# Kernel optimization log

Measured on AMD Instinct MI355X. Metric: run time of the kernel, lower is better.

The kernel has to match this reference:

```python
import jax, jax.numpy as jnp
import numpy as np

B = 2097152  # number of Gaussians


def setup_inputs() -> dict:
    key = jax.random.key(0)
    k1, k2, k3, k4, k5, k6 = jax.random.split(key, 6)
    return {
        "loc1": jax.random.normal(k1, (B, 3), dtype=jnp.float32),
        "scale1": jax.random.uniform(k2, (B, 3), dtype=jnp.float32),
        "rot_matrix1": jax.random.normal(k3, (B, 3, 3), dtype=jnp.float32),
        "loc2": jax.random.normal(k4, (B, 3), dtype=jnp.float32),
        "scale2": jax.random.uniform(k5, (B, 3), dtype=jnp.float32),
        "rot_matrix2": jax.random.normal(k6, (B, 3, 3), dtype=jnp.float32),
    }


def reference(loc1, scale1, rot_matrix1, loc2, scale2, rot_matrix2):
    # ||mu1 - mu2||^2  -> (B,)
    loc_diff2 = jnp.sum((loc1 - loc2) ** 2, axis=-1)

    # cov2 = R2 diag(scale2) R2^T  -> (B,3,3)
    cov2 = jnp.einsum("bij,bj,bkj->bik", rot_matrix2, scale2, rot_matrix2)
    # cov2 rotated into frame of Gaussian 1: R1^T cov2 R1  -> (B,3,3)
    cov2_R1 = jnp.einsum("bji,bjk,bkl->bil", rot_matrix1, cov2, rot_matrix1)

    # E = diag(sqrt(s1)) cov2_R1 diag(sqrt(s1)), then symmetrize
    s1_sqrt = jnp.sqrt(scale1)  # (B,3)
    E = s1_sqrt[:, :, None] * cov2_R1 * s1_sqrt[:, None, :]
    E = (E + jnp.swapaxes(E, 1, 2)) * 0.5

    # trace of matrix sqrt via eigenvalues: sum (lambda^2)^(1/4) = sum |lambda|^(1/2)
    E_eig = jnp.linalg.eigvalsh(E)  # (B,3)
    E_sqrt_trace = jnp.sum(jnp.sqrt(jnp.sqrt(E_eig ** 2)), axis=-1)

    cov_wasserstein = jnp.sum(scale1, axis=-1) + jnp.sum(scale2, axis=-1) - 2.0 * E_sqrt_trace
    cov_wasserstein = jnp.maximum(cov_wasserstein, 0.0)
    return jnp.sqrt(loc_diff2 + cov_wasserstein)
```

## Files before the change

### kernel.cpp

```cpp
#include <hip/hip_runtime.h>
#include <math.h>

#define BLK 256

typedef __attribute__((address_space(1))) void gvoid_t;
typedef __attribute__((address_space(3))) void lvoid_t;

__device__ __forceinline__ void lds_dma16(const float* gsrc, float* ldst) {
    __builtin_amdgcn_global_load_lds((gvoid_t*)gsrc, (lvoid_t*)ldst, 16, 0, 0);
}
__device__ __forceinline__ void lds_dma4(const float* gsrc, float* ldst) {
    __builtin_amdgcn_global_load_lds((gvoid_t*)gsrc, (lvoid_t*)ldst, 4, 0, 0);
}

struct F3 { float x, y, z; };

__global__ __launch_bounds__(BLK, 8) void wasserstein_kernel(
    const float* __restrict__ loc1,   const float* __restrict__ scale1,
    const float* __restrict__ rot1,   const float* __restrict__ loc2,
    const float* __restrict__ scale2, const float* __restrict__ rot2,
    float* __restrict__ out)
{
    __shared__ __align__(16) float smem[4 * 1152];

    const int tid  = threadIdx.x;
    const int lane = tid & 63;
    const int wave = tid >> 6;
    const long long blockStart = (long long)blockIdx.x * BLK;
    const long long waveStart  = blockStart + (long long)(wave * 64);

    float* wR1 = smem + wave * 1152;
    float* wR2 = wR1 + 576;

    {
        const float* g1 = rot1 + waveStart * 9;
        const float* g2 = rot2 + waveStart * 9;
        lds_dma16(g1 + lane * 4,       wR1);
        lds_dma16(g1 + 256 + lane * 4, wR1 + 256);
        lds_dma4 (g1 + 512 + lane,     wR1 + 512);
        lds_dma16(g2 + lane * 4,       wR2);
        lds_dma16(g2 + 256 + lane * 4, wR2 + 256);
        lds_dma4 (g2 + 512 + lane,     wR2 + 512);
    }

    const long long i = blockStart + tid;
    const F3 L1 = *reinterpret_cast<const F3*>(loc1   + i * 3);
    const F3 L2 = *reinterpret_cast<const F3*>(loc2   + i * 3);
    const F3 S1 = *reinterpret_cast<const F3*>(scale1 + i * 3);
    const F3 S2 = *reinterpret_cast<const F3*>(scale2 + i * 3);

    const float dx = L1.x - L2.x, dy = L1.y - L2.y, dz = L1.z - L2.z;
    const float loc_diff2 = dx * dx + dy * dy + dz * dz;
    const float s1a = S1.x, s1b = S1.y, s1c = S1.z;
    const float s2a = S2.x, s2b = S2.y, s2c = S2.z;

    asm volatile("s_waitcnt vmcnt(0)" ::: "memory");
    __builtin_amdgcn_sched_barrier(0);

    float R1[9], R2[9];
#pragma unroll
    for (int k = 0; k < 9; ++k) R1[k] = wR1[lane * 9 + k];
#pragma unroll
    for (int k = 0; k < 9; ++k) R2[k] = wR2[lane * 9 + k];

    const float m00 = s2a * R2[0] * R2[0] + s2b * R2[1] * R2[1] + s2c * R2[2] * R2[2];
    const float m01 = s2a * R2[0] * R2[3] + s2b * R2[1] * R2[4] + s2c * R2[2] * R2[5];
    const float m02 = s2a * R2[0] * R2[6] + s2b * R2[1] * R2[7] + s2c * R2[2] * R2[8];
    const float m11 = s2a * R2[3] * R2[3] + s2b * R2[4] * R2[4] + s2c * R2[5] * R2[5];
    const float m12 = s2a * R2[3] * R2[6] + s2b * R2[4] * R2[7] + s2c * R2[5] * R2[8];
    const float m22 = s2a * R2[6] * R2[6] + s2b * R2[7] * R2[7] + s2c * R2[8] * R2[8];

    float A[9];
    A[0] = m00 * R1[0] + m01 * R1[3] + m02 * R1[6];
    A[1] = m00 * R1[1] + m01 * R1[4] + m02 * R1[7];
    A[2] = m00 * R1[2] + m01 * R1[5] + m02 * R1[8];
    A[3] = m01 * R1[0] + m11 * R1[3] + m12 * R1[6];
    A[4] = m01 * R1[1] + m11 * R1[4] + m12 * R1[7];
    A[5] = m01 * R1[2] + m11 * R1[5] + m12 * R1[8];
    A[6] = m02 * R1[0] + m12 * R1[3] + m22 * R1[6];
    A[7] = m02 * R1[1] + m12 * R1[4] + m22 * R1[7];
    A[8] = m02 * R1[2] + m12 * R1[5] + m22 * R1[8];

    float T[9];
    T[0] = R1[0] * A[0] + R1[3] * A[3] + R1[6] * A[6];
    T[1] = R1[0] * A[1] + R1[3] * A[4] + R1[6] * A[7];
    T[2] = R1[0] * A[2] + R1[3] * A[5] + R1[6] * A[8];
    T[3] = R1[1] * A[0] + R1[4] * A[3] + R1[7] * A[6];
    T[4] = R1[1] * A[1] + R1[4] * A[4] + R1[7] * A[7];
    T[5] = R1[1] * A[2] + R1[4] * A[5] + R1[7] * A[8];
    T[6] = R1[2] * A[0] + R1[5] * A[3] + R1[8] * A[6];
    T[7] = R1[2] * A[1] + R1[5] * A[4] + R1[8] * A[7];
    T[8] = R1[2] * A[2] + R1[5] * A[5] + R1[8] * A[8];

    const float sq0 = sqrtf(s1a), sq1 = sqrtf(s1b), sq2 = sqrtf(s1c);
    const float e00 = s1a * T[0];
    const float e11 = s1b * T[4];
    const float e22 = s1c * T[8];
    const float e01 = 0.5f * sq0 * sq1 * (T[1] + T[3]);
    const float e02 = 0.5f * sq0 * sq2 * (T[2] + T[6]);
    const float e12 = 0.5f * sq1 * sq2 * (T[5] + T[7]);

    const float q  = (e00 + e11 + e22) * (1.0f / 3.0f);
    const float p1 = e01 * e01 + e02 * e02 + e12 * e12;
    const float d0 = e00 - q, d1 = e11 - q, d2 = e22 - q;
    const float p2 = d0 * d0 + d1 * d1 + d2 * d2 + 2.0f * p1;

    float trace_sqrt;
    if (p2 > 1e-24f) {
        const float p   = sqrtf(p2 * (1.0f / 6.0f));
        const float inv = 1.0f / p;
        const float b00 = d0 * inv, b11 = d1 * inv, b22 = d2 * inv;
        const float b01 = e01 * inv, b02 = e02 * inv, b12 = e12 * inv;
        float detB = b00 * (b11 * b22 - b12 * b12)
                   - b01 * (b01 * b22 - b12 * b02)
                   + b02 * (b01 * b12 - b11 * b02);
        float r = 0.5f * detB;
        r = fminf(fmaxf(r, -1.0f), 1.0f);
        const float phi  = acosf(r) * (1.0f / 3.0f);
        const float twop = 2.0f * p;
        const float eig1 = q + twop * cosf(phi);
        const float eig3 = q + twop * cosf(phi + 2.0943951023931953f);
        const float eig2 = 3.0f * q - eig1 - eig3;
        trace_sqrt = sqrtf(fabsf(eig1)) + sqrtf(fabsf(eig2)) + sqrtf(fabsf(eig3));
    } else {
        trace_sqrt = 3.0f * sqrtf(fabsf(q));
    }

    float cov_w = (s1a + s1b + s1c) + (s2a + s2b + s2c) - 2.0f * trace_sqrt;
    cov_w = fmaxf(cov_w, 0.0f);
    out[i] = sqrtf(loc_diff2 + cov_w);
}

extern "C" void kernel_launch(void* const* d_in, const int* in_sizes, int n_in,
                              void* d_out, int out_size, void* d_ws, size_t ws_size,
                              hipStream_t stream) {
    const float* loc1   = (const float*)d_in[0];
    const float* scale1 = (const float*)d_in[1];
    const float* rot1   = (const float*)d_in[2];
    const float* loc2   = (const float*)d_in[3];
    const float* scale2 = (const float*)d_in[4];
    const float* rot2   = (const float*)d_in[5];
    float* out = (float*)d_out;

    const int B = in_sizes[0] / 3;
    const int grid = B / BLK;

    wasserstein_kernel<<<grid, BLK, 0, stream>>>(loc1, scale1, rot1,
                                                 loc2, scale2, rot2, out);
}
```

Before: 238.7 us.

## Use persistent grid-stride kernel with software-pipelined loads and fast math intrinsics

Replaces the one-element-per-thread launch, which staged rotation matrices through LDS DMA, with a fixed 1024-block grid-stride kernel. Each thread loads its next element while computing the current one, aiming to hide memory latency. Global loads are now plain per-thread strided scalar loads instead of coalesced LDS staging, which may hurt coalescing. acosf is replaced by a polynomial approximation and sqrt, rcp, sin and cos by hardware intrinsics, trading some accuracy for fewer instructions.

```diff
diff --git a/kernel.cpp b/kernel.cpp
--- a/kernel.cpp
+++ b/kernel.cpp
@@ -1,67 +1,43 @@
 #include <hip/hip_runtime.h>
 #include <math.h>
 
-#define BLK 256
+#define BLK  256
+#define GRID 1024
 
-typedef __attribute__((address_space(1))) void gvoid_t;
-typedef __attribute__((address_space(3))) void lvoid_t;
+struct Elem {
+    float l1x, l1y, l1z, l2x, l2y, l2z;
+    float s1a, s1b, s1c, s2a, s2b, s2c;
+    float R1[9], R2[9];
+};
 
-__device__ __forceinline__ void lds_dma16(const float* gsrc, float* ldst) {
-    __builtin_amdgcn_global_load_lds((gvoid_t*)gsrc, (lvoid_t*)ldst, 16, 0, 0);
-}
-__device__ __forceinline__ void lds_dma4(const float* gsrc, float* ldst) {
-    __builtin_amdgcn_global_load_lds((gvoid_t*)gsrc, (lvoid_t*)ldst, 4, 0, 0);
+__device__ __forceinline__ void load_elem(
+    Elem& e, long long i,
+    const float* __restrict__ loc1, const float* __restrict__ scale1,
+    const float* __restrict__ rot1, const float* __restrict__ loc2,
+    const float* __restrict__ scale2, const float* __restrict__ rot2)
+{
+    const float* p;
+    p = loc1 + i * 3;   e.l1x = p[0]; e.l1y = p[1]; e.l1z = p[2];
+    p = loc2 + i * 3;   e.l2x = p[0]; e.l2y = p[1]; e.l2z = p[2];
+    p = scale1 + i * 3; e.s1a = p[0]; e.s1b = p[1]; e.s1c = p[2];
+    p = scale2 + i * 3; e.s2a = p[0]; e.s2b = p[1]; e.s2c = p[2];
+    p = rot1 + i * 9;
+#pragma unroll
+    for (int k = 0; k < 9; ++k) e.R1[k] = p[k];
+    p = rot2 + i * 9;
+#pragma unroll
+    for (int k = 0; k < 9; ++k) e.R2[k] = p[k];
 }
 
-struct F3 { float x, y, z; };
+__device__ __forceinline__ float compute_elem(const Elem& e)
+{
+    const float dx = e.l1x - e.l2x, dy = e.l1y - e.l2y, dz = e.l1z - e.l2z;
+    const float loc_diff2 = dx * dx + dy * dy + dz * dz;
 
-__global__ __launch_bounds__(BLK, 8) void wasserstein_kernel(
-    const float* __restrict__ loc1,   const float* __restrict__ scale1,
-    const float* __restrict__ rot1,   const float* __restrict__ loc2,
-    const float* __restrict__ scale2, const float* __restrict__ rot2,
-    float* __restrict__ out)
-{
-    __shared__ __align__(16) float smem[4 * 1152];
-
-    const int tid  = threadIdx.x;
-    const int lane = tid & 63;
-    const int wave = tid >> 6;
-    const long long blockStart = (long long)blockIdx.x * BLK;
-    const long long waveStart  = blockStart + (long long)(wave * 64);
-
-    float* wR1 = smem + wave * 1152;
-    float* wR2 = wR1 + 576;
-
-    {
-        const float* g1 = rot1 + waveStart * 9;
-        const float* g2 = rot2 + waveStart * 9;
-        lds_dma16(g1 + lane * 4,       wR1);
-        lds_dma16(g1 + 256 + lane * 4, wR1 + 256);
-        lds_dma4 (g1 + 512 + lane,     wR1 + 512);
-        lds_dma16(g2 + lane * 4,       wR2);
-        lds_dma16(g2 + 256 + lane * 4, wR2 + 256);
-        lds_dma4 (g2 + 512 + lane,     wR2 + 512);
-    }
-
-    const long long i = blockStart + tid;
-    const F3 L1 = *reinterpret_cast<const F3*>(loc1   + i * 3);
-    const F3 L2 = *reinterpret_cast<const F3*>(loc2   + i * 3);
-    const F3 S1 = *reinterpret_cast<const F3*>(scale1 + i * 3);
-    const F3 S2 = *reinterpret_cast<const F3*>(scale2 + i * 3);
-
-    const float dx = L1.x - L2.x, dy = L1.y - L2.y, dz = L1.z - L2.z;
-    const float loc_diff2 = dx * dx + dy * dy + dz * dz;
-    const float s1a = S1.x, s1b = S1.y, s1c = S1.z;
-    const float s2a = S2.x, s2b = S2.y, s2c = S2.z;
-
-    asm volatile("s_waitcnt vmcnt(0)" ::: "memory");
-    __builtin_amdgcn_sched_barrier(0);
-
-    float R1[9], R2[9];
-#pragma unroll
-    for (int k = 0; k < 9; ++k) R1[k] = wR1[lane * 9 + k];
-#pragma unroll
-    for (int k = 0; k < 9; ++k) R2[k] = wR2[lane * 9 + k];
+    const float s1a = e.s1a, s1b = e.s1b, s1c = e.s1c;
+    const float s2a = e.s2a, s2b = e.s2b, s2c = e.s2c;
+    const float* R1 = e.R1;
+    const float* R2 = e.R2;
 
     const float m00 = s2a * R2[0] * R2[0] + s2b * R2[1] * R2[1] + s2c * R2[2] * R2[2];
     const float m01 = s2a * R2[0] * R2[3] + s2b * R2[1] * R2[4] + s2c * R2[2] * R2[5];
@@ -92,7 +68,9 @@
     T[7] = R1[2] * A[1] + R1[5] * A[4] + R1[8] * A[7];
     T[8] = R1[2] * A[2] + R1[5] * A[5] + R1[8] * A[8];
 
-    const float sq0 = sqrtf(s1a), sq1 = sqrtf(s1b), sq2 = sqrtf(s1c);
+    const float sq0 = __builtin_amdgcn_sqrtf(s1a);
+    const float sq1 = __builtin_amdgcn_sqrtf(s1b);
+    const float sq2 = __builtin_amdgcn_sqrtf(s1c);
     const float e00 = s1a * T[0];
     const float e11 = s1b * T[4];
     const float e22 = s1c * T[8];
@@ -107,8 +85,8 @@
 
     float trace_sqrt;
     if (p2 > 1e-24f) {
-        const float p   = sqrtf(p2 * (1.0f / 6.0f));
-        const float inv = 1.0f / p;
+        const float p   = __builtin_amdgcn_sqrtf(p2 * (1.0f / 6.0f));
+        const float inv = __builtin_amdgcn_rcpf(p);
         const float b00 = d0 * inv, b11 = d1 * inv, b22 = d2 * inv;
         const float b01 = e01 * inv, b02 = e02 * inv, b12 = e12 * inv;
         float detB = b00 * (b11 * b22 - b12 * b12)
@@ -116,19 +94,63 @@
                    + b02 * (b01 * b12 - b11 * b02);
         float r = 0.5f * detB;
         r = fminf(fmaxf(r, -1.0f), 1.0f);
-        const float phi  = acosf(r) * (1.0f / 3.0f);
+
+        const float ax = fabsf(r);
+        const float z  = __builtin_amdgcn_sqrtf(1.0f - ax);
+        const float w  = z * (1.5707288f + ax * (-0.2121144f
+                           + ax * (0.0742610f + ax * (-0.0187293f))));
+        const float ac = (r >= 0.0f) ? w : (3.14159265358979f - w);
+
+        const float phi = ac * (1.0f / 3.0f);
+        const float c   = __cosf(phi);
+        const float s   = __sinf(phi);
         const float twop = 2.0f * p;
-        const float eig1 = q + twop * cosf(phi);
-        const float eig3 = q + twop * cosf(phi + 2.0943951023931953f);
+        const float eig1 = q + twop * c;
+        const float eig3 = q + twop * (-0.5f * c - 0.86602540378f * s);
         const float eig2 = 3.0f * q - eig1 - eig3;
-        trace_sqrt = sqrtf(fabsf(eig1)) + sqrtf(fabsf(eig2)) + sqrtf(fabsf(eig3));
+        trace_sqrt = __builtin_amdgcn_sqrtf(fabsf(eig1))
+                   + __builtin_amdgcn_sqrtf(fabsf(eig2))
+                   + __builtin_amdgcn_sqrtf(fabsf(eig3));
     } else {
-        trace_sqrt = 3.0f * sqrtf(fabsf(q));
+        trace_sqrt = 3.0f * __builtin_amdgcn_sqrtf(fabsf(q));
     }
 
     float cov_w = (s1a + s1b + s1c) + (s2a + s2b + s2c) - 2.0f * trace_sqrt;
     cov_w = fmaxf(cov_w, 0.0f);
-    out[i] = sqrtf(loc_diff2 + cov_w);
+    return __builtin_amdgcn_sqrtf(loc_diff2 + cov_w);
+}
+
+__global__ __launch_bounds__(BLK, 4) void wasserstein_kernel(
+    const float* __restrict__ loc1,   const float* __restrict__ scale1,
+    const float* __restrict__ rot1,   const float* __restrict__ loc2,
+    const float* __restrict__ scale2, const float* __restrict__ rot2,
+    float* __restrict__ out, int B)
+{
+    const long long stride = (long long)GRID * BLK;
+    long long idx = (long long)blockIdx.x * BLK + threadIdx.x;
+    const int nPer = B / (GRID * BLK);
+
+    if ((nPer & 1) == 0 && nPer >= 2) {
+        Elem a, b;
+        load_elem(a, idx, loc1, scale1, rot1, loc2, scale2, rot2);
+        const int pairs = nPer >> 1;
+        for (int p = 0; p < pairs - 1; ++p) {
+            load_elem(b, idx + stride, loc1, scale1, rot1, loc2, scale2, rot2);
+            out[idx] = compute_elem(a);
+            load_elem(a, idx + 2 * stride, loc1, scale1, rot1, loc2, scale2, rot2);
+            out[idx + stride] = compute_elem(b);
+            idx += 2 * stride;
+        }
+        load_elem(b, idx + stride, loc1, scale1, rot1, loc2, scale2, rot2);
+        out[idx] = compute_elem(a);
+        out[idx + stride] = compute_elem(b);
+    } else {
+        for (long long i = idx; i < B; i += stride) {
+            Elem a;
+            load_elem(a, i, loc1, scale1, rot1, loc2, scale2, rot2);
+            out[i] = compute_elem(a);
+        }
+    }
 }
 
 extern "C" void kernel_launch(void* const* d_in, const int* in_sizes, int n_in,
@@ -143,8 +165,7 @@
     float* out = (float*)d_out;
 
     const int B = in_sizes[0] / 3;
-    const int grid = B / BLK;
 
-    wasserstein_kernel<<<grid, BLK, 0, stream>>>(loc1, scale1, rot1,
-                                                 loc2, scale2, rot2, out);
+    wasserstein_kernel<<<GRID, BLK, 0, stream>>>(loc1, scale1, rot1,
+                                                 loc2, scale2, rot2, out, B);
 }
```

Result: no change. 242.2 us (+1.5%).
